# Kernel tuning notes

Hardware: AMD Instinct MI355X
Metric: run time of the kernel (lower is better)

## Reference

```python
import jax, jax.numpy as jnp
import numpy as np

B, T, E = 2, 2048, 2048
H = 16
DH = E // H  # 128
FFN = 4 * E  # 8192
EPS = 1e-5


def _layernorm(x, g, b):
    mu = jnp.mean(x, axis=-1, keepdims=True)
    var = jnp.mean((x - mu) ** 2, axis=-1, keepdims=True)
    return (x - mu) * jax.lax.rsqrt(var + EPS) * g + b


def setup_inputs() -> dict:
    key = jax.random.key(0)
    ks = jax.random.split(key, 8)
    s = 0.02
    return {
        "x": jax.random.normal(ks[0], (B, T, E), jnp.float32),
        "g1": jnp.ones((E,), jnp.float32),
        "b1": jnp.zeros((E,), jnp.float32),
        "wq": jax.random.normal(ks[1], (E, E), jnp.float32) * s,
        "wk": jax.random.normal(ks[2], (E, E), jnp.float32) * s,
        "wv": jax.random.normal(ks[3], (E, E), jnp.float32) * s,
        "wo": jax.random.normal(ks[4], (E, E), jnp.float32) * s,
        "g2": jnp.ones((E,), jnp.float32),
        "b2": jnp.zeros((E,), jnp.float32),
        "w1": jax.random.normal(ks[5], (E, FFN), jnp.float32) * s,
        "w2": jax.random.normal(ks[6], (E, FFN), jnp.float32) * s,
        "w3": jax.random.normal(ks[7], (FFN, E), jnp.float32) * s,
    }


def reference(x, g1, b1, wq, wk, wv, wo, g2, b2, w1, w2, w3):
    Bx, Tx, Ex = x.shape
    # --- attention block (pre-LN, residual) ---
    h = _layernorm(x, g1, b1)
    q = (h @ wq).reshape(Bx, Tx, H, DH)
    k = (h @ wk).reshape(Bx, Tx, H, DH)
    v = (h @ wv).reshape(Bx, Tx, H, DH)
    scores = jnp.einsum('bqhd,bkhd->bhqk', q, k) / jnp.sqrt(jnp.float32(DH))
    causal = jnp.tril(jnp.ones((Tx, Tx), bool))  # [T,T]
    scores = jnp.where(causal[None, None], scores, -jnp.inf)
    attn = jax.nn.softmax(scores, axis=-1)
    ctx = jnp.einsum('bhqk,bkhd->bqhd', attn, v).reshape(Bx, Tx, H * DH)
    x = x + ctx @ wo
    # --- SwiGLU MLP block (pre-LN, residual) ---
    h = _layernorm(x, g2, b2)
    gated = jax.nn.silu(h @ w1) * (h @ w2)
    return x + gated @ w3
```

## Files before the change

### kernel.cpp

```cpp
#include <hip/hip_runtime.h>


#define T_SEQ 2048
#define E_DIM 2048
#define N_HEAD 16
#define D_HEAD 128
#define FFN_DIM 8192
#define M_ROWS 4096
#define QS (3 * E_DIM)

typedef unsigned short u16;
typedef short short8 __attribute__((ext_vector_type(8)));
typedef float f32x4 __attribute__((ext_vector_type(4)));

#define DEV __device__ __forceinline__

DEV u16 f2bf(float f) {
  unsigned u = __float_as_uint(f);
  u += 0x7fffu + ((u >> 16) & 1u);
  return (u16)(u >> 16);
}
DEV float bf2f(u16 h) { return __uint_as_float(((unsigned)h) << 16); }

DEV void async16(void* lds, const void* g) {
  __builtin_amdgcn_global_load_lds((const __attribute__((address_space(1))) void*)g,
                                   (__attribute__((address_space(3))) void*)lds, 16, 0, 0);
}

__global__ __launch_bounds__(256) void ln_kernel(const float* __restrict__ x,
                                                 const float* __restrict__ gw,
                                                 const float* __restrict__ bw,
                                                 u16* __restrict__ out) {
  int row = blockIdx.x;
  int t = threadIdx.x;
  const float4* xr = (const float4*)(x + (size_t)row * E_DIM);
  float4 a = xr[t], c = xr[t + 256];
  float s = a.x + a.y + a.z + a.w + c.x + c.y + c.z + c.w;
  float q = a.x * a.x + a.y * a.y + a.z * a.z + a.w * a.w +
            c.x * c.x + c.y * c.y + c.z * c.z + c.w * c.w;
  for (int off = 32; off > 0; off >>= 1) {
    s += __shfl_down(s, off);
    q += __shfl_down(q, off);
  }
  __shared__ float red[8];
  if ((t & 63) == 0) { red[(t >> 6) * 2] = s; red[(t >> 6) * 2 + 1] = q; }
  __syncthreads();
  s = red[0] + red[2] + red[4] + red[6];
  q = red[1] + red[3] + red[5] + red[7];
  float mu = s * (1.f / E_DIM);
  float rs = rsqrtf(q * (1.f / E_DIM) - mu * mu + 1e-5f);
  const float4* g4 = (const float4*)gw;
  const float4* b4 = (const float4*)bw;
  float4 g0 = g4[t], g1v = g4[t + 256], e0 = b4[t], e1 = b4[t + 256];
  ushort4 o0, o1;
  o0.x = f2bf((a.x - mu) * rs * g0.x + e0.x);
  o0.y = f2bf((a.y - mu) * rs * g0.y + e0.y);
  o0.z = f2bf((a.z - mu) * rs * g0.z + e0.z);
  o0.w = f2bf((a.w - mu) * rs * g0.w + e0.w);
  o1.x = f2bf((c.x - mu) * rs * g1v.x + e1.x);
  o1.y = f2bf((c.y - mu) * rs * g1v.y + e1.y);
  o1.z = f2bf((c.z - mu) * rs * g1v.z + e1.z);
  o1.w = f2bf((c.w - mu) * rs * g1v.w + e1.w);
  ((ushort4*)(out + (size_t)row * E_DIM))[t] = o0;
  ((ushort4*)(out + (size_t)row * E_DIM))[t + 256] = o1;
}

__global__ __launch_bounds__(256) void cvt_t_kernel(const float* __restrict__ W,
                                                    u16* __restrict__ WT,
                                                    int Kd, int Nd) {
  __shared__ float tile[32][33];
  int tx = threadIdx.x, ty = threadIdx.y;
  int n0 = blockIdx.x * 32, k0 = blockIdx.y * 32;
#pragma unroll
  for (int i = 0; i < 4; i++)
    tile[ty + i * 8][tx] = W[(size_t)(k0 + ty + i * 8) * Nd + n0 + tx];
  __syncthreads();
#pragma unroll
  for (int i = 0; i < 4; i++)
    WT[(size_t)(n0 + ty + i * 8) * Kd + k0 + tx] = f2bf(tile[tx][ty + i * 8]);
}

__global__ __launch_bounds__(256) void transpose_v_kernel(const u16* __restrict__ qkv,
                                                          u16* __restrict__ vt) {
  __shared__ u16 tile[32][33];
  int tx = threadIdx.x, ty = threadIdx.y;
  int b = blockIdx.z;
  int t0 = blockIdx.x * 32, e0 = blockIdx.y * 32;
#pragma unroll
  for (int i = 0; i < 4; i++)
    tile[ty + i * 8][tx] =
        qkv[(size_t)(b * T_SEQ + t0 + ty + i * 8) * QS + 2 * E_DIM + e0 + tx];
  __syncthreads();
#pragma unroll
  for (int i = 0; i < 4; i++)
    vt[((size_t)b * E_DIM + e0 + ty + i * 8) * T_SEQ + t0 + tx] = tile[tx][ty + i * 8];
}

template <int MODE>
__global__ __launch_bounds__(512, 1) void gemm8p(const u16* __restrict__ A,
                                                 const u16* __restrict__ BT,
                                                 void* __restrict__ Cout,
                                                 const void* __restrict__ Extra,
                                                 int N, int K, int colMajorXcd) {
  __shared__ u16 Abuf[2 * 2 * 256 * 32];
  __shared__ u16 Bbuf[2 * 2 * 256 * 32];
  const int t = threadIdx.x;
  const int w = t >> 6, l = t & 63, g = l >> 4, lq = l & 15;
  const int wm = w >> 2, wn = w & 3;

  const int gx = gridDim.x, gy = gridDim.y;
  const int nwg = gx * gy;
  int lin = colMajorXcd ? (blockIdx.x * gy + blockIdx.y)
                        : (blockIdx.y * gx + blockIdx.x);
  const int qq = nwg >> 3;
  int wg = (lin & 7) * qq + (lin >> 3);
  int bx, by;
  if (colMajorXcd) { bx = wg / gy; by = wg - bx * gy; }
  else             { by = wg / gx; bx = wg - by * gx; }
  const size_t bm = (size_t)by * 256, bn = (size_t)bx * 256;

  const int srow = l >> 2;
  const int sswz = (((l & 3) ^ ((srow ^ (srow >> 2)) & 3)) << 3);
  const int rdswz = ((g ^ ((lq ^ (lq >> 2)) & 3)) << 3);
  const u16* aS0 = A + (bm + w * 16 + srow) * (size_t)K + sswz;
  const u16* aS1 = A + (bm + 128 + w * 16 + srow) * (size_t)K + sswz;
  const u16* bS0 = BT + (bn + w * 16 + srow) * (size_t)K + sswz;
  const u16* bS1 = BT + (bn + 128 + w * 16 + srow) * (size_t)K + sswz;

#define STA8(DB, KS, TILE)                                                   \
  {                                                                          \
    size_t off_ = (size_t)(TILE) * 64 + (KS) * 32;                           \
    async16(Abuf + (DB) * 16384 + (KS) * 8192 + w * 512, aS0 + off_);        \
    async16(Abuf + (DB) * 16384 + (KS) * 8192 + 4096 + w * 512, aS1 + off_); \
  }
#define STB8(DB, KS, TILE)                                                   \
  {                                                                          \
    size_t off_ = (size_t)(TILE) * 64 + (KS) * 32;                           \
    async16(Bbuf + (DB) * 16384 + (KS) * 8192 + w * 512, bS0 + off_);        \
    async16(Bbuf + (DB) * 16384 + (KS) * 8192 + 4096 + w * 512, bS1 + off_); \
  }
#define RDA8(DB, KS, MH)                                                     \
  _Pragma("unroll") for (int mm = 0; mm < 4; ++mm)                           \
      af[mm] = *(const short8*)(Abuf + (DB) * 16384 + (KS) * 8192 +          \
                                (wm * 128 + (MH) * 64 + mm * 16 + lq) * 32 + \
                                rdswz);
#define RDB8(DB, KS)                                                         \
  _Pragma("unroll") for (int nn = 0; nn < 4; ++nn)                           \
      bf[nn] = *(const short8*)(Bbuf + (DB) * 16384 + (KS) * 8192 +          \
                                (wn * 64 + nn * 16 + lq) * 32 + rdswz);
#define MM168(MH)                                                            \
  _Pragma("unroll") for (int mm = 0; mm < 4; ++mm)                           \
      _Pragma("unroll") for (int nn = 0; nn < 4; ++nn)                       \
          acc[(MH) * 4 + mm][nn] = __builtin_amdgcn_mfma_f32_16x16x32_bf16(  \
              af[mm], bf[nn], acc[(MH) * 4 + mm][nn], 0, 0, 0);
#define SYNCA                                                                \
  asm volatile("s_barrier" ::: "memory");                                    \
  asm volatile("s_waitcnt lgkmcnt(0)" ::: "memory");                         \
  __builtin_amdgcn_sched_barrier(0);                                         \
  __builtin_amdgcn_s_setprio(1);
#define ENDP                                                                 \
  __builtin_amdgcn_s_setprio(0);
#define BAR2 asm volatile("s_barrier" ::: "memory");

  const int NT = K >> 6, NI = NT >> 1;
  f32x4 acc[8][4] = {};
  short8 af[4], bf[4];

  STA8(0, 0, 0); STB8(0, 0, 0);
  STA8(0, 1, 0); STB8(0, 1, 0);
  STA8(1, 0, 1); STB8(1, 0, 1);
  asm volatile("s_waitcnt vmcnt(4)" ::: "memory");
  BAR2;

  for (int j = 0; j < NI; ++j) {
    const int t1 = 2 * j + 1, t2 = 2 * j + 2, t3 = 2 * j + 3;
    const bool s2 = t2 < NT, s3 = t3 < NT;
    RDB8(0, 0); RDA8(0, 0, 0);
    STA8(1, 1, t1);
    SYNCA; MM168(0); ENDP; BAR2;
    RDA8(0, 0, 1);
    STB8(1, 1, t1);
    SYNCA; MM168(1); ENDP; BAR2;
    RDB8(0, 1); RDA8(0, 1, 0);
    if (s2) STA8(0, 0, t2);
    SYNCA; MM168(0); ENDP; BAR2;
    RDA8(0, 1, 1);
    if (s2) STB8(0, 0, t2);
    SYNCA; MM168(1); ENDP;
    if (j + 1 == NI) asm volatile("s_waitcnt vmcnt(0)" ::: "memory");
    else             asm volatile("s_waitcnt vmcnt(4)" ::: "memory");
    BAR2;
    RDB8(1, 0); RDA8(1, 0, 0);
    if (s2) STA8(0, 1, t2);
    SYNCA; MM168(0); ENDP; BAR2;
    RDA8(1, 0, 1);
    if (s2) STB8(0, 1, t2);
    SYNCA; MM168(1); ENDP; BAR2;
    RDB8(1, 1); RDA8(1, 1, 0);
    if (s3) STA8(1, 0, t3);
    SYNCA; MM168(0); ENDP; BAR2;
    RDA8(1, 1, 1);
    if (s3) STB8(1, 0, t3);
    SYNCA; MM168(1); ENDP;
    asm volatile("s_waitcnt vmcnt(4)" ::: "memory");
    BAR2;
  }
#undef STA8
#undef STB8
#undef RDA8
#undef RDB8
#undef MM168
#undef SYNCA
#undef ENDP
#undef BAR2

#pragma unroll
  for (int m = 0; m < 8; m++) {
    size_t row = bm + wm * 128 + m * 16 + 4 * g;
#pragma unroll
    for (int n = 0; n < 4; n++) {
      size_t col = bn + wn * 64 + n * 16 + lq;
#pragma unroll
      for (int r = 0; r < 4; r++) {
        size_t idx = (row + r) * (size_t)N + col;
        if constexpr (MODE == 0) {
          ((u16*)Cout)[idx] = f2bf(acc[m][n][r]);
        } else if constexpr (MODE == 1) {
          ((float*)Cout)[idx] = ((const float*)Extra)[idx] + acc[m][n][r];
        } else {
          float a = bf2f(((const u16*)Extra)[idx]);
          float sil = a / (1.f + exp2f(-1.4426950408889634f * a));
          ((u16*)Cout)[idx] = f2bf(sil * acc[m][n][r]);
        }
      }
    }
  }
}

__global__ __launch_bounds__(256, 3) void attn_kernel(const u16* __restrict__ QKV,
                                                      const u16* __restrict__ VT,
                                                      u16* __restrict__ CTX) {
  __shared__ u16 Ks[64 * 128];
  __shared__ u16 Vs[128 * 64];
  __shared__ u16 P_all[4][16 * 72];
  const int t = threadIdx.x;
  const int w = t >> 6, l = t & 63, g = l >> 4, lq = l & 15;
  u16* P = P_all[w];
  const int q0blk = blockIdx.x * 64;
  const int q0w = q0blk + w * 16;
  const int bh = blockIdx.y, b = bh >> 4, h = bh & 15;
  const u16* qp = QKV + (size_t)b * T_SEQ * QS + h * D_HEAD;
  const u16* kp = QKV + (size_t)b * T_SEQ * QS + E_DIM + h * D_HEAD;
  const u16* vp = VT + ((size_t)b * E_DIM + h * D_HEAD) * T_SEQ;

  short8 qf[4];
#pragma unroll
  for (int ks = 0; ks < 4; ks++)
    qf[ks] = *(const short8*)(qp + (size_t)(q0w + lq) * QS + ks * 32 + g * 8);

  f32x4 acc[8] = {};
  float m2[4], ls[4];
#pragma unroll
  for (int r = 0; r < 4; r++) { m2[r] = -1e30f; ls[r] = 0.f; }
  const float sc = 0.08838834764831845f * 1.4426950408889634f;

  const int kRow0 = 16 * w + (l >> 4);
  const int kChunk = l & 15;
  const int vRow0 = 32 * w + (l >> 3);
  const int vChunk = l & 7;

  for (int kv0 = 0; kv0 <= q0blk; kv0 += 64) {
#pragma unroll
    for (int j = 0; j < 4; j++) {
      int R = kRow0 + 4 * j;
      async16(Ks + (16 * w + 4 * j) * 128,
              kp + (size_t)(kv0 + R) * QS + ((kChunk ^ (R & 7)) << 3));
    }
#pragma unroll
    for (int j = 0; j < 4; j++) {
      int D = vRow0 + 8 * j;
      async16(Vs + (32 * w + 8 * j) * 64,
              vp + (size_t)D * T_SEQ + kv0 + ((vChunk ^ (D & 7)) << 3));
    }
    __syncthreads();

    f32x4 s[4];
#pragma unroll
    for (int ct = 0; ct < 4; ct++) {
      s[ct] = f32x4{0.f, 0.f, 0.f, 0.f};
#pragma unroll
      for (int ks = 0; ks < 4; ks++) {
        short8 kf = *(const short8*)(Ks + (ct * 16 + lq) * 128 +
                                     (((ks * 4 + g) ^ (lq & 7)) << 3));
        s[ct] = __builtin_amdgcn_mfma_f32_16x16x32_bf16(qf[ks], kf, s[ct], 0, 0, 0);
      }
    }
    float sv[4][4];
#pragma unroll
    for (int ct = 0; ct < 4; ct++)
#pragma unroll
      for (int r = 0; r < 4; r++) sv[ct][r] = s[ct][r] * sc;
    if (kv0 + 64 > q0w) {
#pragma unroll
      for (int ct = 0; ct < 4; ct++)
#pragma unroll
        for (int r = 0; r < 4; r++)
          if (kv0 + ct * 16 + lq > q0w + 4 * g + r) sv[ct][r] = -1e30f;
    }
    float mx[4];
#pragma unroll
    for (int r = 0; r < 4; r++)
      mx[r] = fmaxf(fmaxf(sv[0][r], sv[1][r]), fmaxf(sv[2][r], sv[3][r]));
#pragma unroll
    for (int off = 1; off < 16; off <<= 1)
#pragma unroll
      for (int r = 0; r < 4; r++) mx[r] = fmaxf(mx[r], __shfl_xor(mx[r], off));
#pragma unroll
    for (int r = 0; r < 4; r++) {
      float mn = fmaxf(m2[r], mx[r]);
      float sca = exp2f(m2[r] - mn);
      m2[r] = mn;
      float sum = 0.f;
#pragma unroll
      for (int ct = 0; ct < 4; ct++) {
        float pv = exp2f(sv[ct][r] - mn);
        sum += pv;
        P[(4 * g + r) * 72 + ct * 16 + lq] = f2bf(pv);
      }
      ls[r] = ls[r] * sca + sum;
#pragma unroll
      for (int n = 0; n < 8; n++) acc[n][r] *= sca;
    }
    short8 pa[2];
#pragma unroll
    for (int ks2 = 0; ks2 < 2; ks2++)
      pa[ks2] = *(const short8*)(P + lq * 72 + ks2 * 32 + g * 8);
#pragma unroll
    for (int n = 0; n < 8; n++)
#pragma unroll
      for (int ks2 = 0; ks2 < 2; ks2++) {
        short8 vf = *(const short8*)(Vs + (n * 16 + lq) * 64 +
                                     (((ks2 * 4 + g) ^ (lq & 7)) << 3));
        acc[n] = __builtin_amdgcn_mfma_f32_16x16x32_bf16(pa[ks2], vf, acc[n], 0, 0, 0);
      }
    __syncthreads();
  }

#pragma unroll
  for (int off = 1; off < 16; off <<= 1)
#pragma unroll
    for (int r = 0; r < 4; r++) ls[r] += __shfl_xor(ls[r], off);
  float inv[4];
#pragma unroll
  for (int r = 0; r < 4; r++) inv[r] = 1.f / ls[r];
  u16* cp = CTX + ((size_t)b * T_SEQ + q0w) * E_DIM + h * D_HEAD;
#pragma unroll
  for (int n = 0; n < 8; n++)
#pragma unroll
    for (int r = 0; r < 4; r++)
      cp[(size_t)(4 * g + r) * E_DIM + n * 16 + lq] = f2bf(acc[n][r] * inv[r]);
}

extern "C" void kernel_launch(void* const* d_in, const int* in_sizes, int n_in,
                              void* d_out, int out_size, void* d_ws, size_t ws_size,
                              hipStream_t stream) {
  (void)in_sizes; (void)n_in; (void)out_size; (void)ws_size;
  const float* x  = (const float*)d_in[0];
  const float* g1 = (const float*)d_in[1];
  const float* b1 = (const float*)d_in[2];
  const float* wq = (const float*)d_in[3];
  const float* wk = (const float*)d_in[4];
  const float* wv = (const float*)d_in[5];
  const float* wo = (const float*)d_in[6];
  const float* g2 = (const float*)d_in[7];
  const float* b2 = (const float*)d_in[8];
  const float* w1 = (const float*)d_in[9];
  const float* w2 = (const float*)d_in[10];
  const float* w3 = (const float*)d_in[11];
  float* out = (float*)d_out;

  const size_t EE2 = (size_t)E_DIM * E_DIM * 2;
  const size_t EF2 = (size_t)E_DIM * FFN_DIM * 2;
  const size_t ME2 = (size_t)M_ROWS * E_DIM * 2;
  char* p = (char*)d_ws;
  u16* wqkvT = (u16*)p; p += 3 * EE2;
  u16* woT = (u16*)p; p += EE2;
  u16* w1T = (u16*)p; p += EF2;
  u16* w2T = (u16*)p; p += EF2;
  u16* w3T = (u16*)p; p += EF2;
  u16* Hb  = (u16*)p; p += ME2;
  u16* QKVb = (u16*)p; p += (size_t)M_ROWS * QS * 2;
  u16* VTb = (u16*)p; p += ME2;
  u16* CTXb = (u16*)p; p += ME2;
  u16* U1b = QKVb;

  dim3 blk32(32, 8);
  cvt_t_kernel<<<dim3(E_DIM / 32, E_DIM / 32), blk32, 0, stream>>>(wq, wqkvT, E_DIM, E_DIM);
  cvt_t_kernel<<<dim3(E_DIM / 32, E_DIM / 32), blk32, 0, stream>>>(wk, wqkvT + E_DIM * E_DIM, E_DIM, E_DIM);
  cvt_t_kernel<<<dim3(E_DIM / 32, E_DIM / 32), blk32, 0, stream>>>(wv, wqkvT + 2 * E_DIM * E_DIM, E_DIM, E_DIM);
  cvt_t_kernel<<<dim3(E_DIM / 32, E_DIM / 32), blk32, 0, stream>>>(wo, woT, E_DIM, E_DIM);
  cvt_t_kernel<<<dim3(FFN_DIM / 32, E_DIM / 32), blk32, 0, stream>>>(w1, w1T, E_DIM, FFN_DIM);
  cvt_t_kernel<<<dim3(FFN_DIM / 32, E_DIM / 32), blk32, 0, stream>>>(w2, w2T, E_DIM, FFN_DIM);
  cvt_t_kernel<<<dim3(E_DIM / 32, FFN_DIM / 32), blk32, 0, stream>>>(w3, w3T, FFN_DIM, E_DIM);

  ln_kernel<<<M_ROWS, 256, 0, stream>>>(x, g1, b1, Hb);
  gemm8p<0><<<dim3(QS / 256, M_ROWS / 256), 512, 0, stream>>>(Hb, wqkvT, QKVb, nullptr, QS, E_DIM, 1);
  transpose_v_kernel<<<dim3(T_SEQ / 32, E_DIM / 32, 2), blk32, 0, stream>>>(QKVb, VTb);
  attn_kernel<<<dim3(T_SEQ / 64, 2 * N_HEAD), 256, 0, stream>>>(QKVb, VTb, CTXb);
  gemm8p<1><<<dim3(E_DIM / 256, M_ROWS / 256), 512, 0, stream>>>(CTXb, woT, out, x, E_DIM, E_DIM, 0);

  ln_kernel<<<M_ROWS, 256, 0, stream>>>(out, g2, b2, Hb);
  gemm8p<0><<<dim3(FFN_DIM / 256, M_ROWS / 256), 512, 0, stream>>>(Hb, w1T, U1b, nullptr, FFN_DIM, E_DIM, 1);
  gemm8p<2><<<dim3(FFN_DIM / 256, M_ROWS / 256), 512, 0, stream>>>(Hb, w2T, U1b, U1b, FFN_DIM, E_DIM, 1);
  gemm8p<1><<<dim3(E_DIM / 256, M_ROWS / 256), 512, 0, stream>>>(U1b, w3T, out, out, E_DIM, FFN_DIM, 0);
}
```

Baseline: 1.021 ms.

## Template GEMM on M tile size, use 128-row tiles for narrow GEMMs

Parameterises the pipelined bf16 GEMM by its M tile size and launches 128x256 tiles for the QKV, output-projection and down-projection GEMMs, keeping 256x256 for the wide FFN up-projections. The aim is more workgroups on the narrow GEMMs, which at 256x256 launch only 128 or 384 blocks and leave CUs idle or unevenly loaded. It also changes the LDS staging layout and swizzle (interleaved row pairs with a new read offset) and switches the narrow GEMMs to column-major XCD ordering. In exchange, the smaller tiles lower arithmetic intensity per block and double B-tile traffic for those GEMMs.

```diff
diff --git a/kernel.cpp b/kernel.cpp
--- a/kernel.cpp
+++ b/kernel.cpp
@@ -96,14 +96,17 @@
     vt[((size_t)b * E_DIM + e0 + ty + i * 8) * T_SEQ + t0 + tx] = tile[tx][ty + i * 8];
 }
 
-template <int MODE>
+template <int MODE, int BM_>
 __global__ __launch_bounds__(512, 1) void gemm8p(const u16* __restrict__ A,
                                                  const u16* __restrict__ BT,
                                                  void* __restrict__ Cout,
                                                  const void* __restrict__ Extra,
                                                  int N, int K, int colMajorXcd) {
-  __shared__ u16 Abuf[2 * 2 * 256 * 32];
-  __shared__ u16 Bbuf[2 * 2 * 256 * 32];
+  constexpr int MM = BM_ / 64;
+  constexpr int AUNIT = BM_ * 32;
+  constexpr int VC = (BM_ == 256) ? 4 : 3;
+  __shared__ u16 Abuf[4 * AUNIT];
+  __shared__ u16 Bbuf[4 * 8192];
   const int t = threadIdx.x;
   const int w = t >> 6, l = t & 63, g = l >> 4, lq = l & 15;
   const int wm = w >> 2, wn = w & 3;
@@ -117,59 +120,61 @@
   int bx, by;
   if (colMajorXcd) { bx = wg / gy; by = wg - bx * gy; }
   else             { by = wg / gx; bx = wg - by * gx; }
-  const size_t bm = (size_t)by * 256, bn = (size_t)bx * 256;
-
-  const int srow = l >> 2;
-  const int sswz = (((l & 3) ^ ((srow ^ (srow >> 2)) & 3)) << 3);
-  const int rdswz = ((g ^ ((lq ^ (lq >> 2)) & 3)) << 3);
-  const u16* aS0 = A + (bm + w * 16 + srow) * (size_t)K + sswz;
-  const u16* aS1 = A + (bm + 128 + w * 16 + srow) * (size_t)K + sswz;
-  const u16* bS0 = BT + (bn + w * 16 + srow) * (size_t)K + sswz;
-  const u16* bS1 = BT + (bn + 128 + w * 16 + srow) * (size_t)K + sswz;
-
-#define STA8(DB, KS, TILE)                                                   \
-  {                                                                          \
-    size_t off_ = (size_t)(TILE) * 64 + (KS) * 32;                           \
-    async16(Abuf + (DB) * 16384 + (KS) * 8192 + w * 512, aS0 + off_);        \
-    async16(Abuf + (DB) * 16384 + (KS) * 8192 + 4096 + w * 512, aS1 + off_); \
-  }
-#define STB8(DB, KS, TILE)                                                   \
-  {                                                                          \
-    size_t off_ = (size_t)(TILE) * 64 + (KS) * 32;                           \
-    async16(Bbuf + (DB) * 16384 + (KS) * 8192 + w * 512, bS0 + off_);        \
-    async16(Bbuf + (DB) * 16384 + (KS) * 8192 + 4096 + w * 512, bS1 + off_); \
-  }
-#define RDA8(DB, KS, MH)                                                     \
-  _Pragma("unroll") for (int mm = 0; mm < 4; ++mm)                           \
-      af[mm] = *(const short8*)(Abuf + (DB) * 16384 + (KS) * 8192 +          \
-                                (wm * 128 + (MH) * 64 + mm * 16 + lq) * 32 + \
-                                rdswz);
-#define RDB8(DB, KS)                                                         \
-  _Pragma("unroll") for (int nn = 0; nn < 4; ++nn)                           \
-      bf[nn] = *(const short8*)(Bbuf + (DB) * 16384 + (KS) * 8192 +          \
-                                (wn * 64 + nn * 16 + lq) * 32 + rdswz);
-#define MM168(MH)                                                            \
-  _Pragma("unroll") for (int mm = 0; mm < 4; ++mm)                           \
-      _Pragma("unroll") for (int nn = 0; nn < 4; ++nn)                       \
-          acc[(MH) * 4 + mm][nn] = __builtin_amdgcn_mfma_f32_16x16x32_bf16(  \
-              af[mm], bf[nn], acc[(MH) * 4 + mm][nn], 0, 0, 0);
-#define SYNCA                                                                \
-  asm volatile("s_barrier" ::: "memory");                                    \
-  asm volatile("s_waitcnt lgkmcnt(0)" ::: "memory");                         \
-  __builtin_amdgcn_sched_barrier(0);                                         \
+  const size_t bm = (size_t)by * BM_, bn = (size_t)bx * 256;
+
+  const int srcrow = ((l >> 3) << 1) | (l & 1);
+  const int csrc = ((((l >> 1) & 3) ^ ((l >> 3) & 3)) << 3);
+  const u16* aSrc = A + (bm + w * 16 + srcrow) * (size_t)K + csrc;
+  const u16* bSrc = BT + (bn + w * 16 + srcrow) * (size_t)K + csrc;
+  const int rdoff = (((lq & 1) + 2 * (g ^ ((lq >> 1) & 3))) << 3);
+
+#define STA8(DB, KS, TILE)                                                    \
+  {                                                                           \
+    u16* Ad = Abuf + (DB) * (2 * AUNIT) + (KS)*AUNIT + w * 512;               \
+    const u16* as_ = aSrc + (size_t)(TILE)*64 + (KS)*32;                      \
+    async16(Ad, as_);                                                         \
+    if constexpr (BM_ == 256) async16(Ad + 4096, as_ + (size_t)128 * K);      \
+  }
+#define STB8(DB, KS, TILE)                                                    \
+  {                                                                           \
+    u16* Bd = Bbuf + (DB)*16384 + (KS)*8192 + w * 512;                        \
+    const u16* bs_ = bSrc + (size_t)(TILE)*64 + (KS)*32;                      \
+    async16(Bd, bs_);                                                         \
+    async16(Bd + 4096, bs_ + (size_t)128 * K);                                \
+  }
+#define RDA8(DB, KS, MH)                                                      \
+  _Pragma("unroll") for (int mm = 0; mm < MM; ++mm)                           \
+      af[mm] = *(const short8*)(Abuf + (DB) * (2 * AUNIT) + (KS)*AUNIT +      \
+                                (wm * (BM_ / 4) + (MH) * (BM_ / 8) + mm * 8 + \
+                                 (lq >> 1)) * 64 + rdoff);
+#define RDB8(DB, KS)                                                          \
+  _Pragma("unroll") for (int nn = 0; nn < 4; ++nn)                            \
+      bf[nn] = *(const short8*)(Bbuf + (DB)*16384 + (KS)*8192 +               \
+                                (wn * 32 + nn * 8 + (lq >> 1)) * 64 + rdoff);
+#define MM168(MH)                                                             \
+  _Pragma("unroll") for (int mm = 0; mm < MM; ++mm)                           \
+      _Pragma("unroll") for (int nn = 0; nn < 4; ++nn)                        \
+          acc[(MH)*MM + mm][nn] = __builtin_amdgcn_mfma_f32_16x16x32_bf16(    \
+              af[mm], bf[nn], acc[(MH)*MM + mm][nn], 0, 0, 0);
+#define SYNCA                                                                 \
+  asm volatile("s_barrier" ::: "memory");                                     \
+  asm volatile("s_waitcnt lgkmcnt(0)" ::: "memory");                          \
+  __builtin_amdgcn_sched_barrier(0);                                          \
   __builtin_amdgcn_s_setprio(1);
-#define ENDP                                                                 \
-  __builtin_amdgcn_s_setprio(0);
+#define ENDP __builtin_amdgcn_s_setprio(0);
 #define BAR2 asm volatile("s_barrier" ::: "memory");
+#define WAITVC                                                                \
+  if constexpr (BM_ == 256) asm volatile("s_waitcnt vmcnt(4)" ::: "memory");  \
+  else                      asm volatile("s_waitcnt vmcnt(3)" ::: "memory");
 
   const int NT = K >> 6, NI = NT >> 1;
-  f32x4 acc[8][4] = {};
-  short8 af[4], bf[4];
+  f32x4 acc[2 * MM][4] = {};
+  short8 af[MM > 4 ? MM : 4], bf[4];
 
   STA8(0, 0, 0); STB8(0, 0, 0);
   STA8(0, 1, 0); STB8(0, 1, 0);
   STA8(1, 0, 1); STB8(1, 0, 1);
-  asm volatile("s_waitcnt vmcnt(4)" ::: "memory");
+  WAITVC;
   BAR2;
 
   for (int j = 0; j < NI; ++j) {
@@ -187,8 +192,8 @@
     RDA8(0, 1, 1);
     if (s2) STB8(0, 0, t2);
     SYNCA; MM168(1); ENDP;
-    if (j + 1 == NI) asm volatile("s_waitcnt vmcnt(0)" ::: "memory");
-    else             asm volatile("s_waitcnt vmcnt(4)" ::: "memory");
+    if (j + 1 == NI) { asm volatile("s_waitcnt vmcnt(0)" ::: "memory"); }
+    else { WAITVC; }
     BAR2;
     RDB8(1, 0); RDA8(1, 0, 0);
     if (s2) STA8(0, 1, t2);
@@ -202,7 +207,7 @@
     RDA8(1, 1, 1);
     if (s3) STB8(1, 0, t3);
     SYNCA; MM168(1); ENDP;
-    asm volatile("s_waitcnt vmcnt(4)" ::: "memory");
+    WAITVC;
     BAR2;
   }
 #undef STA8
@@ -213,10 +218,11 @@
 #undef SYNCA
 #undef ENDP
 #undef BAR2
-
-#pragma unroll
-  for (int m = 0; m < 8; m++) {
-    size_t row = bm + wm * 128 + m * 16 + 4 * g;
+#undef WAITVC
+
+#pragma unroll
+  for (int m = 0; m < 2 * MM; m++) {
+    size_t row = bm + wm * (BM_ / 2) + m * 16 + 4 * g;
 #pragma unroll
     for (int n = 0; n < 4; n++) {
       size_t col = bn + wn * 64 + n * 16 + lq;
@@ -404,13 +410,13 @@
   cvt_t_kernel<<<dim3(E_DIM / 32, FFN_DIM / 32), blk32, 0, stream>>>(w3, w3T, FFN_DIM, E_DIM);
 
   ln_kernel<<<M_ROWS, 256, 0, stream>>>(x, g1, b1, Hb);
-  gemm8p<0><<<dim3(QS / 256, M_ROWS / 256), 512, 0, stream>>>(Hb, wqkvT, QKVb, nullptr, QS, E_DIM, 1);
+  gemm8p<0, 128><<<dim3(QS / 256, M_ROWS / 128), 512, 0, stream>>>(Hb, wqkvT, QKVb, nullptr, QS, E_DIM, 1);
   transpose_v_kernel<<<dim3(T_SEQ / 32, E_DIM / 32, 2), blk32, 0, stream>>>(QKVb, VTb);
   attn_kernel<<<dim3(T_SEQ / 64, 2 * N_HEAD), 256, 0, stream>>>(QKVb, VTb, CTXb);
-  gemm8p<1><<<dim3(E_DIM / 256, M_ROWS / 256), 512, 0, stream>>>(CTXb, woT, out, x, E_DIM, E_DIM, 0);
+  gemm8p<1, 128><<<dim3(E_DIM / 256, M_ROWS / 128), 512, 0, stream>>>(CTXb, woT, out, x, E_DIM, E_DIM, 1);
 
   ln_kernel<<<M_ROWS, 256, 0, stream>>>(out, g2, b2, Hb);
-  gemm8p<0><<<dim3(FFN_DIM / 256, M_ROWS / 256), 512, 0, stream>>>(Hb, w1T, U1b, nullptr, FFN_DIM, E_DIM, 1);
-  gemm8p<2><<<dim3(FFN_DIM / 256, M_ROWS / 256), 512, 0, stream>>>(Hb, w2T, U1b, U1b, FFN_DIM, E_DIM, 1);
-  gemm8p<1><<<dim3(E_DIM / 256, M_ROWS / 256), 512, 0, stream>>>(U1b, w3T, out, out, E_DIM, FFN_DIM, 0);
-}
+  gemm8p<0, 256><<<dim3(FFN_DIM / 256, M_ROWS / 256), 512, 0, stream>>>(Hb, w1T, U1b, nullptr, FFN_DIM, E_DIM, 1);
+  gemm8p<2, 256><<<dim3(FFN_DIM / 256, M_ROWS / 256), 512, 0, stream>>>(Hb, w2T, U1b, U1b, FFN_DIM, E_DIM, 1);
+  gemm8p<1, 128><<<dim3(E_DIM / 256, M_ROWS / 128), 512, 0, stream>>>(U1b, w3T, out, out, E_DIM, FFN_DIM, 1);
+}
```

Measured after the change: 957.2 us. 6.3% less time.
